# Optimization experiments

Hardware: AMD Instinct MI355X
Metric: run time of the kernel (lower is better)

## Reference

```python
import jax, jax.numpy as jnp
import numpy as np

B, N, M, D, F, L = 128, 512, 512, 256, 512, 5
EPS = 1e-5  # torch InstanceNorm1d default eps


def setup_inputs() -> dict:
    key = jax.random.key(0)
    ks = jax.random.split(key, 12)
    s_d = 1.0 / np.sqrt(D)
    s_f = 1.0 / np.sqrt(F)
    return {
        "row_emb": jax.random.normal(ks[0], (B, N, D), jnp.float32),
        "col_emb": jax.random.normal(ks[1], (B, M, D), jnp.float32),
        "cost_mat": jax.random.uniform(ks[2], (B, N, M), jnp.float32),
        "log_scale": jnp.float32(np.log2(N)),
        "Wq": jax.random.normal(ks[3], (L, 2, D, D), jnp.float32) * s_d,
        "Wk": jax.random.normal(ks[4], (L, 2, D, D), jnp.float32) * s_d,
        "Wv": jax.random.normal(ks[5], (L, 2, D, D), jnp.float32) * s_d,
        "g1": jnp.ones((L, 2, D), jnp.float32),
        "be1": jnp.zeros((L, 2, D), jnp.float32),
        "W1": jax.random.normal(ks[6], (L, 2, D, F), jnp.float32) * s_d,
        "b1": jnp.zeros((L, 2, F), jnp.float32),
        "W2": jax.random.normal(ks[7], (L, 2, F, D), jnp.float32) * s_f,
        "b2": jnp.zeros((L, 2, D), jnp.float32),
        "g2": jnp.ones((L, 2, D), jnp.float32),
        "be2": jnp.zeros((L, 2, D), jnp.float32),
        "alpha": jnp.ones((L, 2), jnp.float32),
    }


def _instance_norm(x, g, b):
    # x: (B, seq, D); normalize over seq per (batch, channel), affine over D
    mu = x.mean(axis=1, keepdims=True)
    var = jnp.mean(jnp.square(x - mu), axis=1, keepdims=True)
    return (x - mu) * jax.lax.rsqrt(var + EPS) * g + b


def _aft(q, k, v, adaptation_bias):
    # Attention-free mixing: exp(bias) shared across numerator/denominator GEMMs
    E = jnp.exp(adaptation_bias)          # (B, n, m)
    ek = jnp.exp(k)                       # (B, m, D)
    num = jnp.einsum('bnm,bmd->bnd', E, ek * v)
    den = jnp.einsum('bnm,bmd->bnd', E, ek)
    weighted = jnp.nan_to_num(num / den)  # matches torch nan/inf safety net
    return jax.nn.sigmoid(q) * weighted


def _enc_block(xr, xc, cm, Wq, Wk, Wv, g1, be1, W1, b1, W2, b2, g2, be2, alpha):
    q = xr @ Wq
    k = xc @ Wk
    v = xc @ Wv
    out_aft = _aft(q, k, v, alpha * cm)
    h1 = _instance_norm(xr + out_aft, g1, be1)
    ff = jax.nn.relu(h1 @ W1 + b1) @ W2 + b2
    return _instance_norm(h1 + ff, g2, be2)


def reference(row_emb, col_emb, cost_mat, log_scale, Wq, Wk, Wv,
              g1, be1, W1, b1, W2, b2, g2, be2, alpha):
    cm = (-log_scale) * cost_mat          # (B, N, M)
    cmT = jnp.swapaxes(cm, 1, 2)          # (B, M, N)
    for l in range(L):
        new_row = _enc_block(row_emb, col_emb, cm,
                             Wq[l, 0], Wk[l, 0], Wv[l, 0], g1[l, 0], be1[l, 0],
                             W1[l, 0], b1[l, 0], W2[l, 0], b2[l, 0],
                             g2[l, 0], be2[l, 0], alpha[l, 0])
        new_col = _enc_block(col_emb, row_emb, cmT,
                             Wq[l, 1], Wk[l, 1], Wv[l, 1], g1[l, 1], be1[l, 1],
                             W1[l, 1], b1[l, 1], W2[l, 1], b2[l, 1],
                             g2[l, 1], be2[l, 1], alpha[l, 1])
        row_emb, col_emb = new_row, new_col
    return (row_emb, col_emb)
```

## Files before the change

### kernel.cpp

```cpp
#include <hip/hip_runtime.h>

typedef unsigned short u16;
typedef __attribute__((ext_vector_type(8))) short short8;
typedef __attribute__((ext_vector_type(4))) float f32x4;

#define DEVFUN __device__ __forceinline__

namespace {

constexpr int kB = 128;
constexpr int kN = 512;
constexpr int kD = 256;
constexpr int kF = 512;
constexpr int kL = 5;
constexpr float kEPS = 1e-5f;
constexpr long BND = (long)kB * kN * kD;

DEVFUN float bf2f(u16 u) {
  unsigned v = ((unsigned)u) << 16;
  float f;
  __builtin_memcpy(&f, &v, 4);
  return f;
}
DEVFUN u16 f2bf(float f) {
  unsigned x;
  __builtin_memcpy(&x, &f, 4);
  x = (x + 0x7FFFu + ((x >> 16) & 1u)) >> 16;
  return (u16)x;
}
DEVFUN u16 f2h(float f) {
  _Float16 h = (_Float16)f;
  u16 u;
  __builtin_memcpy(&u, &h, 2);
  return u;
}
DEVFUN float h2f(u16 u) {
  _Float16 h;
  __builtin_memcpy(&h, &u, 2);
  return (float)h;
}
DEVFUN float fsig(float x) { return 1.f / (1.f + __expf(-x)); }

union Pk8 { u16 p[8]; uint4 v; };
union Pk4 { u16 p[4]; uint2 v; };

DEVFUN void gload16(const u16* g, u16* l) {
  __builtin_amdgcn_global_load_lds(
      (const __attribute__((address_space(1))) void*)g,
      (__attribute__((address_space(3))) void*)l, 16, 0, 0);
}

DEVFUN void waitv8() { asm volatile("s_waitcnt vmcnt(8)" ::: "memory"); }
DEVFUN void waitv0() { asm volatile("s_waitcnt vmcnt(0)" ::: "memory"); }

template <int MODE>
__global__ __launch_bounds__(256) void tcvt(const float* __restrict__ src,
                                            u16* __restrict__ dst, int R,
                                            int C, const float* __restrict__ al,
                                            int pi, const float* __restrict__ ls) {
  __shared__ u16 T[64 * 64];
  const int t = threadIdx.x;
  const long z = blockIdx.z;
  const int cBase = blockIdx.x * 64, rBase = blockIdx.y * 64;
  float s = 0.f;
  if constexpr (MODE == 1) s = -al[pi] * ls[0];
#pragma unroll
  for (int i = 0; i < 4; ++i) {
    int u = i * 256 + t;
    int n = u >> 4, m4 = u & 15;
    float4 v = *(const float4*)(src + (z * R + rBase + n) * C + cBase + m4 * 4);
    Pk4 pk;
    if constexpr (MODE == 1) {
      pk.p[0] = f2bf(__expf(s * v.x)); pk.p[1] = f2bf(__expf(s * v.y));
      pk.p[2] = f2bf(__expf(s * v.z)); pk.p[3] = f2bf(__expf(s * v.w));
    } else if constexpr (MODE == 2) {
      pk.p[0] = f2h(v.x); pk.p[1] = f2h(v.y);
      pk.p[2] = f2h(v.z); pk.p[3] = f2h(v.w);
    } else {
      pk.p[0] = f2bf(v.x); pk.p[1] = f2bf(v.y);
      pk.p[2] = f2bf(v.z); pk.p[3] = f2bf(v.w);
    }
    int ch = (m4 >> 1) ^ ((n >> 3) & 7), hf = m4 & 1;
    *(uint2*)&T[n * 64 + ch * 8 + hf * 4] = pk.v;
  }
  __syncthreads();
#pragma unroll
  for (int j = 0; j < 2; ++j) {
    int u = j * 256 + t;
    int om = u >> 3, nc = u & 7;
    Pk8 pk;
#pragma unroll
    for (int i = 0; i < 8; ++i) {
      int n = nc * 8 + i;
      int ch = (om >> 3) ^ ((n >> 3) & 7);
      pk.p[i] = T[n * 64 + ch * 8 + (om & 7)];
    }
    *(uint4*)(dst + (z * C + cBase + om) * R + rBase + nc * 8) = pk.v;
  }
}

__global__ __launch_bounds__(256) void eexp(const float* __restrict__ src,
                                            u16* __restrict__ dst, long n8,
                                            const float* __restrict__ al,
                                            int pi, const float* __restrict__ ls) {
  const float s = -al[pi] * ls[0];
  for (long i = blockIdx.x * 256 + threadIdx.x; i < n8;
       i += (long)gridDim.x * 256) {
    const float* p = src + i * 8;
    float4 v0 = *(const float4*)p, v1 = *(const float4*)(p + 4);
    Pk8 pk;
    pk.p[0] = f2bf(__expf(s * v0.x)); pk.p[1] = f2bf(__expf(s * v0.y));
    pk.p[2] = f2bf(__expf(s * v0.z)); pk.p[3] = f2bf(__expf(s * v0.w));
    pk.p[4] = f2bf(__expf(s * v1.x)); pk.p[5] = f2bf(__expf(s * v1.y));
    pk.p[6] = f2bf(__expf(s * v1.z)); pk.p[7] = f2bf(__expf(s * v1.w));
    *(uint4*)(dst + i * 8) = pk.v;
  }
}

__global__ __launch_bounds__(256) void eexpH(const u16* __restrict__ src,
                                             u16* __restrict__ dst, long n8,
                                             const float* __restrict__ al,
                                             int pi, const float* __restrict__ ls) {
  const float s = -al[pi] * ls[0];
  for (long i = blockIdx.x * 256 + threadIdx.x; i < n8;
       i += (long)gridDim.x * 256) {
    Pk8 h;
    h.v = *(const uint4*)(src + i * 8);
    Pk8 pk;
#pragma unroll
    for (int q = 0; q < 8; ++q) pk.p[q] = f2bf(__expf(s * h2f(h.p[q])));
    *(uint4*)(dst + i * 8) = pk.v;
  }
}

template <int MODE>
__global__ __launch_bounds__(256) void cvtb(const float* __restrict__ src,
                                            u16* __restrict__ dst, long n8) {
  for (long i = blockIdx.x * 256 + threadIdx.x; i < n8;
       i += (long)gridDim.x * 256) {
    const float* p = src + i * 8;
    float4 v0 = *(const float4*)p, v1 = *(const float4*)(p + 4);
    Pk8 pk;
    if constexpr (MODE == 2) {
      pk.p[0] = f2h(v0.x); pk.p[1] = f2h(v0.y);
      pk.p[2] = f2h(v0.z); pk.p[3] = f2h(v0.w);
      pk.p[4] = f2h(v1.x); pk.p[5] = f2h(v1.y);
      pk.p[6] = f2h(v1.z); pk.p[7] = f2h(v1.w);
    } else {
      pk.p[0] = f2bf(v0.x); pk.p[1] = f2bf(v0.y);
      pk.p[2] = f2bf(v0.z); pk.p[3] = f2bf(v0.w);
      pk.p[4] = f2bf(v1.x); pk.p[5] = f2bf(v1.y);
      pk.p[6] = f2bf(v1.z); pk.p[7] = f2bf(v1.w);
    }
    *(uint4*)(dst + i * 8) = pk.v;
  }
}

DEVFUN void mfma_step(const u16* As, const u16* Bs, int wr, int wc, int lr,
                      int lhi, f32x4 acc[4][4]) {
#pragma unroll
  for (int ks = 0; ks < 2; ++ks) {
    short8 af[4], bfr[4];
#pragma unroll
    for (int m = 0; m < 4; ++m) {
      int r = wr + m * 16 + lr;
      af[m] = *(const short8*)&As[r * 64 + (((ks << 2) + lhi) ^ (r & 7)) * 8];
    }
#pragma unroll
    for (int n = 0; n < 4; ++n) {
      int r = wc + n * 16 + lr;
      bfr[n] = *(const short8*)&Bs[r * 64 + (((ks << 2) + lhi) ^ (r & 7)) * 8];
    }
#pragma unroll
    for (int m = 0; m < 4; ++m)
#pragma unroll
      for (int n = 0; n < 4; ++n)
        acc[m][n] = __builtin_amdgcn_mfma_f32_16x16x32_bf16(af[m], bfr[n],
                                                            acc[m][n], 0, 0, 0);
  }
}

enum Epi { EP_SIG = 0, EP_RELUB, EP_BIASRES };

template <int EPI, int KK>
__global__ __launch_bounds__(256) void gemm_mf(
    const u16* __restrict__ Asrc, const u16* __restrict__ WT, int gx,
    void* __restrict__ outp, const void* __restrict__ aux,
    const u16* __restrict__ aux2b, float* __restrict__ statsF) {
  __shared__ u16 SM[4 * 8192];
  const int t = threadIdx.x;
  const int lane = t & 63, wid = t >> 6;
  const int lr = lane & 15, lhi = lane >> 4;
  const int wr = (wid >> 1) * 64, wc = (wid & 1) * 64;
  const int cpx = gridDim.x >> 3;
  const int rb = (blockIdx.x & 7) * cpx + (blockIdx.x >> 3);
  const int bx = rb % gx;
  const long rowBase = (long)(rb / gx) * 128;
  const int colBase = bx * 128;
  const int r0 = wid * 32;
  const int rl = lane >> 3, sl = lane & 7;

  f32x4 acc[4][4];
#pragma unroll
  for (int m = 0; m < 4; ++m)
#pragma unroll
    for (int n = 0; n < 4; ++n) acc[m][n] = {0.f, 0.f, 0.f, 0.f};

  auto stage = [&](int tt, int pb) {
    const int kt = tt << 6;
    u16* As = SM + pb * 16384;
    u16* Bs = SM + pb * 16384 + 8192;
#pragma unroll
    for (int j = 0; j < 4; ++j) {
      int r = r0 + j * 8 + rl;
      int gch = sl ^ (r & 7);
      gload16(Asrc + (rowBase + r) * KK + kt + gch * 8, &As[(r0 + j * 8) * 64]);
      gload16(WT + (long)(colBase + r) * KK + kt + gch * 8,
              &Bs[(r0 + j * 8) * 64]);
    }
  };

  constexpr int NT = KK >> 6;
  stage(0, 0);
  stage(1, 1);
  waitv8();
  __builtin_amdgcn_s_barrier();
#pragma unroll
  for (int tt = 0; tt < NT - 1; ++tt) {
    mfma_step(SM + (tt & 1) * 16384, SM + (tt & 1) * 16384 + 8192, wr, wc, lr,
              lhi, acc);
    __builtin_amdgcn_s_barrier();
    if (tt + 2 < NT) {
      stage(tt + 2, tt & 1);
      waitv8();
    } else {
      waitv0();
    }
    __builtin_amdgcn_s_barrier();
  }
  mfma_step(SM + ((NT - 1) & 1) * 16384, SM + ((NT - 1) & 1) * 16384 + 8192,
            wr, wc, lr, lhi, acc);

  float psum[4] = {0.f, 0.f, 0.f, 0.f}, psq[4] = {0.f, 0.f, 0.f, 0.f};
#pragma unroll
  for (int m = 0; m < 4; ++m) {
#pragma unroll
    for (int n = 0; n < 4; ++n) {
#pragma unroll
      for (int rr = 0; rr < 4; ++rr) {
        float v = acc[m][n][rr];
        long grow = rowBase + wr + m * 16 + lhi * 4 + rr;
        int gcol = colBase + wc + n * 16 + lr;
        if constexpr (EPI == EP_SIG) {
          ((u16*)outp)[grow * 256 + gcol] = f2bf(fsig(v));
        } else if constexpr (EPI == EP_RELUB) {
          float bb = ((const float*)aux)[gcol];
          ((u16*)outp)[grow * 512 + gcol] = f2bf(fmaxf(v + bb, 0.f));
        } else {
          float bb = ((const float*)aux)[gcol];
          float y = v + bb + bf2f(aux2b[grow * 256 + gcol]);
          ((u16*)outp)[grow * 256 + gcol] = f2bf(y);
          psum[n] += y;
          psq[n] += y * y;
        }
      }
    }
  }

  if constexpr (EPI == EP_BIASRES) {
    __syncthreads();
    float* stS = (float*)SM;
    float* stQ = stS + 8 * 128;
    const int ctr = (wid >> 1) * 4 + lhi;
#pragma unroll
    for (int n = 0; n < 4; ++n) {
      stS[ctr * 128 + wc + n * 16 + lr] = psum[n];
      stQ[ctr * 128 + wc + n * 16 + lr] = psq[n];
    }
    __syncthreads();
    if (t < 128) {
      float s = 0.f, q = 0.f;
#pragma unroll
      for (int i = 0; i < 8; ++i) {
        s += stS[i * 128 + t];
        q += stQ[i * 128 + t];
      }
      const long b = rowBase >> 9;
      const int rblk = (int)((rowBase >> 7) & 3);
      const long o = ((b * 4 + rblk) * 256 + colBase + t) * 2;
      statsF[o] = s;
      statsF[o + 1] = q;
    }
  }
}

union KvSm {
  struct { u16 A[128 * 64]; u16 Bk[128 * 64]; u16 Bv[128 * 64]; } s;
  u16 T[128 * 128];
};

__global__ __launch_bounds__(256) void kv_mf(const u16* __restrict__ Asrc,
                                             const u16* __restrict__ WkT,
                                             const u16* __restrict__ WvT,
                                             u16* __restrict__ Cb) {
  __shared__ KvSm sm;
  const int t = threadIdx.x;
  const int lane = t & 63, wid = t >> 6;
  const int lr = lane & 15, lhi = lane >> 4;
  const int wr = (wid >> 1) * 64, wc = (wid & 1) * 64;
  const int cpx = gridDim.x >> 3;
  const int rb = (blockIdx.x & 7) * cpx + (blockIdx.x >> 3);
  const long rowBase = (long)(rb >> 1) * 128;
  const int colBase = (rb & 1) * 128;
  const long b = rowBase >> 9;
  const int mInB = (int)(rowBase & 511);
  const int r0 = wid * 32;
  const int rl = lane >> 3, sl = lane & 7;

  f32x4 ka[4][4], va[4][4];
#pragma unroll
  for (int m = 0; m < 4; ++m)
#pragma unroll
    for (int n = 0; n < 4; ++n) {
      ka[m][n] = {0.f, 0.f, 0.f, 0.f};
      va[m][n] = {0.f, 0.f, 0.f, 0.f};
    }

  for (int kt = 0; kt < 256; kt += 64) {
#pragma unroll
    for (int j = 0; j < 4; ++j) {
      int r = r0 + j * 8 + rl;
      int gch = sl ^ (r & 7);
      gload16(Asrc + (rowBase + r) * 256 + kt + gch * 8,
              &sm.s.A[(r0 + j * 8) * 64]);
      gload16(WkT + (long)(colBase + r) * 256 + kt + gch * 8,
              &sm.s.Bk[(r0 + j * 8) * 64]);
      gload16(WvT + (long)(colBase + r) * 256 + kt + gch * 8,
              &sm.s.Bv[(r0 + j * 8) * 64]);
    }
    __syncthreads();
    mfma_step(sm.s.A, sm.s.Bk, wr, wc, lr, lhi, ka);
    mfma_step(sm.s.A, sm.s.Bv, wr, wc, lr, lhi, va);
    __syncthreads();
  }

#pragma unroll
  for (int pass = 0; pass < 2; ++pass) {
#pragma unroll
    for (int m = 0; m < 4; ++m) {
#pragma unroll
      for (int n = 0; n < 4; ++n) {
        int m0 = wr + m * 16 + lhi * 4;
        int d = wc + n * 16 + lr;
        Pk4 pk;
#pragma unroll
        for (int rr = 0; rr < 4; ++rr) {
          float ek = __expf(ka[m][n][rr]);
          pk.p[rr] = f2bf(pass ? ek * va[m][n][rr] : ek);
        }
        int slot = (m0 >> 3) ^ (d & 7);
        *(uint2*)&sm.T[d * 128 + slot * 8 + (m0 & 7)] = pk.v;
      }
    }
    __syncthreads();
    const long rbase = b * 512 + (pass ? 0 : 256) + colBase;
#pragma unroll
    for (int j = 0; j < 8; ++j) {
      int idx = j * 256 + t;
      int d = idx >> 4, c = idx & 15;
      uint4 v = *(const uint4*)&sm.T[d * 128 + ((c ^ (d & 7)) * 8)];
      *(uint4*)(Cb + (rbase + d) * 512 + mInB + c * 8) = v;
    }
    __syncthreads();
  }
}

union SmU {
  struct { u16 A[128 * 64]; u16 B[128 * 64]; } s;
  struct { float den[128 * 68]; float st[2][8][64]; } d;
};

__global__ __launch_bounds__(256) void aft_mf(
    const u16* __restrict__ Ebuf, const u16* __restrict__ CbufT,
    const u16* __restrict__ qb, const u16* __restrict__ xrB,
    u16* __restrict__ dst, float* __restrict__ statsF) {
  __shared__ SmU sm;
  const int t = threadIdx.x;
  const int lane = t & 63, wid = t >> 6;
  const int lr = lane & 15, lhi = lane >> 4;
  const int wr = (wid >> 1) * 64, wc = (wid & 1) * 64;
  const int rb = (blockIdx.x & 7) * 256 + (blockIdx.x >> 3);
  const long b = rb >> 4;
  const int nBase = ((rb >> 2) & 3) * 128;
  const int dBase = (rb & 3) * 64;
  const int r0 = wid * 32;
  const int rl = lane >> 3, sl = lane & 7;

  f32x4 acc[4][4];
#pragma unroll
  for (int m = 0; m < 4; ++m)
#pragma unroll
    for (int n = 0; n < 4; ++n) acc[m][n] = {0.f, 0.f, 0.f, 0.f};

  for (int kt = 0; kt < 512; kt += 64) {
#pragma unroll
    for (int j = 0; j < 4; ++j) {
      int r = r0 + j * 8 + rl;
      int gch = sl ^ (r & 7);
      gload16(Ebuf + (b * 512 + nBase + r) * 512 + kt + gch * 8,
              &sm.s.A[(r0 + j * 8) * 64]);
      int gslot = (r < 64) ? (dBase + r) : (256 + dBase + (r - 64));
      gload16(CbufT + (b * 512 + gslot) * 512 + kt + gch * 8,
              &sm.s.B[(r0 + j * 8) * 64]);
    }
    __syncthreads();
    mfma_step(sm.s.A, sm.s.B, wr, wc, lr, lhi, acc);
    __syncthreads();
  }

  if (wc == 64) {
#pragma unroll
    for (int m = 0; m < 4; ++m)
#pragma unroll
      for (int n = 0; n < 4; ++n)
#pragma unroll
        for (int rr = 0; rr < 4; ++rr) {
          int nl = wr + m * 16 + lhi * 4 + rr;
          int dl = n * 16 + lr;
          sm.d.den[nl * 68 + dl] = acc[m][n][rr];
        }
  }
  __syncthreads();
  float psum[4] = {0.f, 0.f, 0.f, 0.f}, psq[4] = {0.f, 0.f, 0.f, 0.f};
  if (wc == 0) {
#pragma unroll
    for (int m = 0; m < 4; ++m)
#pragma unroll
      for (int n = 0; n < 4; ++n)
#pragma unroll
        for (int rr = 0; rr < 4; ++rr) {
          int nl = wr + m * 16 + lhi * 4 + rr;
          int dl = n * 16 + lr;
          float dv = sm.d.den[nl * 68 + dl];
          float w = acc[m][n][rr] / dv;
          if (!(w == w)) w = 0.f;
          else if (w > 3.402823466e38f) w = 3.402823466e38f;
          else if (w < -3.402823466e38f) w = -3.402823466e38f;
          long grow = b * 512 + nBase + nl;
          int gcol = dBase + dl;
          float sq = bf2f(qb[grow * 256 + gcol]);
          float y = bf2f(xrB[grow * 256 + gcol]) + sq * w;
          dst[grow * 256 + gcol] = f2bf(y);
          psum[n] += y;
          psq[n] += y * y;
        }
  }
  __syncthreads();
  if (wc == 0) {
    const int ctr = (wid >> 1) * 4 + lhi;
#pragma unroll
    for (int n = 0; n < 4; ++n) {
      sm.d.st[0][ctr][n * 16 + lr] = psum[n];
      sm.d.st[1][ctr][n * 16 + lr] = psq[n];
    }
  }
  __syncthreads();
  if (t < 64) {
    float s = 0.f, q = 0.f;
#pragma unroll
    for (int i = 0; i < 8; ++i) {
      s += sm.d.st[0][i][t];
      q += sm.d.st[1][i][t];
    }
    const long o = ((b * 4 + (nBase >> 7)) * 256 + dBase + t) * 2;
    statsF[o] = s;
    statsF[o + 1] = q;
  }
}

template <bool LASTF32>
__global__ __launch_bounds__(256) void inormS(const u16* __restrict__ Xin,
                                              const float* __restrict__ stats,
                                              const float* __restrict__ g,
                                              const float* __restrict__ be,
                                              u16* __restrict__ Xb,
                                              float* __restrict__ Xf) {
  const int b = blockIdx.x;
  const int ch0 = blockIdx.y * 64;
  const int nlo = blockIdx.z * 256;
  const int t = threadIdx.x;
  const int lc = t & 63;
  const int ch = ch0 + lc;
  const int nr = t >> 6;
  const long base = (long)b * kN * kD + ch;

  __shared__ float s1[4][64], s2[4][64];
  __shared__ float mu[64], rs[64], gg[64], bb[64];
  {
    const long o = (((long)b * 4 + nr) * 256 + ch) * 2;
    s1[nr][lc] = stats[o];
    s2[nr][lc] = stats[o + 1];
  }
  __syncthreads();
  if (t < 64) {
    float ssum = s1[0][t] + s1[1][t] + s1[2][t] + s1[3][t];
    float ssq = s2[0][t] + s2[1][t] + s2[2][t] + s2[3][t];
    float m = ssum * (1.f / kN);
    float v = ssq * (1.f / kN) - m * m;
    mu[t] = m;
    rs[t] = rsqrtf(v + kEPS);
    gg[t] = g[ch0 + t];
    bb[t] = be[ch0 + t];
  }
  __syncthreads();
  const float m = mu[lc], rr = rs[lc], G = gg[lc], Bt = bb[lc];
  for (int n = nlo + nr; n < nlo + 256; n += 4) {
    long idx = base + (long)n * kD;
    float y = (bf2f(Xin[idx]) - m) * rr * G + Bt;
    Xb[idx] = f2bf(y);
    if constexpr (LASTF32) Xf[idx] = y;
  }
}

}

extern "C" void kernel_launch(void* const* d_in, const int* in_sizes, int n_in,
                              void* d_out, int out_size, void* d_ws,
                              size_t ws_size, hipStream_t stream) {
  (void)in_sizes; (void)n_in; (void)out_size;

  const float* in_row = (const float*)d_in[0];
  const float* in_col = (const float*)d_in[1];
  const float* cost = (const float*)d_in[2];
  const float* lsc = (const float*)d_in[3];
  const float* Wq = (const float*)d_in[4];
  const float* Wk = (const float*)d_in[5];
  const float* Wv = (const float*)d_in[6];
  const float* g1 = (const float*)d_in[7];
  const float* be1 = (const float*)d_in[8];
  const float* W1 = (const float*)d_in[9];
  const float* b1 = (const float*)d_in[10];
  const float* W2 = (const float*)d_in[11];
  const float* b2 = (const float*)d_in[12];
  const float* g2 = (const float*)d_in[13];
  const float* be2 = (const float*)d_in[14];
  const float* alpha = (const float*)d_in[15];

  float* outRow = (float*)d_out;
  float* outCol = outRow + BND;

  u16* qb = (u16*)d_ws;
  u16* h1b = qb;
  u16* CbufT = qb + BND;
  u16* ffmid = CbufT;
  u16* Ebuf = CbufT + 2 * BND;
  u16* bSt = Ebuf + 2 * BND;
  u16* h0b = bSt + 4 * BND;
  u16* h2b = h0b;
  u16* WqT = h0b + BND;
  u16* WkT = WqT + 10L * 256 * 256;
  u16* WvT = WkT + 10L * 256 * 256;
  u16* W1T = WvT + 10L * 256 * 256;
  u16* W2T = W1T + 10L * 512 * 256;
  float* statsF = (float*)(W2T + 10L * 256 * 512);
  u16* costTH = (u16*)(statsF + 128L * 4 * 256 * 2);
  u16* costH = costTH + 2 * BND;
  const long needElems = (long)(costH - (u16*)d_ws) + 2 * BND;
  const bool haveCH = (long)ws_size >= needElems * 2;

  const dim3 blk(256);
  tcvt<0><<<dim3(4, 4, 10), blk, 0, stream>>>(Wq, WqT, 256, 256, nullptr, 0, nullptr);
  tcvt<0><<<dim3(4, 4, 10), blk, 0, stream>>>(Wk, WkT, 256, 256, nullptr, 0, nullptr);
  tcvt<0><<<dim3(4, 4, 10), blk, 0, stream>>>(Wv, WvT, 256, 256, nullptr, 0, nullptr);
  tcvt<0><<<dim3(8, 4, 10), blk, 0, stream>>>(W1, W1T, 256, 512, nullptr, 0, nullptr);
  tcvt<0><<<dim3(4, 8, 10), blk, 0, stream>>>(W2, W2T, 512, 256, nullptr, 0, nullptr);
  cvtb<0><<<1024, blk, 0, stream>>>(in_row, bSt + 0 * BND, BND / 8);
  cvtb<0><<<1024, blk, 0, stream>>>(in_col, bSt + 1 * BND, BND / 8);
  if (haveCH) {
    tcvt<2><<<dim3(8, 8, 128), blk, 0, stream>>>(cost, costTH, 512, 512,
                                                 nullptr, 0, nullptr);
    cvtb<2><<<2048, blk, 0, stream>>>(cost, costH, 2 * BND / 8);
  }

  for (int l = 0; l < kL; ++l) {
    const int inPar = l & 1, outPar = 1 - inPar;
    const u16* bR = bSt + (inPar * 2 + 0) * BND;
    const u16* bC = bSt + (inPar * 2 + 1) * BND;

    for (int side = 0; side < 2; ++side) {
      const u16* xrB = side ? bC : bR;
      const u16* xcB = side ? bR : bC;
      u16* outB = bSt + (outPar * 2 + side) * BND;
      float* outF = side ? outCol : outRow;
      const int pi = l * 2 + side;

      if (side == 0) {
        if (haveCH)
          eexpH<<<4096, blk, 0, stream>>>(costH, Ebuf, 2 * BND / 8, alpha, pi,
                                          lsc);
        else
          eexp<<<4096, blk, 0, stream>>>(cost, Ebuf, 2 * BND / 8, alpha, pi,
                                         lsc);
      } else if (haveCH) {
        eexpH<<<4096, blk, 0, stream>>>(costTH, Ebuf, 2 * BND / 8, alpha, pi,
                                        lsc);
      } else {
        tcvt<1><<<dim3(8, 8, 128), blk, 0, stream>>>(cost, Ebuf, 512, 512,
                                                     alpha, pi, lsc);
      }

      gemm_mf<EP_SIG, 256><<<1024, blk, 0, stream>>>(
          xrB, WqT + (long)pi * 256 * 256, 2, qb, nullptr, nullptr, nullptr);
      kv_mf<<<1024, blk, 0, stream>>>(xcB, WkT + (long)pi * 256 * 256,
                                      WvT + (long)pi * 256 * 256, CbufT);
      aft_mf<<<2048, blk, 0, stream>>>(Ebuf, CbufT, qb, xrB, h0b, statsF);
      inormS<false><<<dim3(128, 4, 2), blk, 0, stream>>>(
          h0b, statsF, g1 + pi * 256, be1 + pi * 256, h1b, nullptr);
      gemm_mf<EP_RELUB, 256><<<2048, blk, 0, stream>>>(
          h1b, W1T + (long)pi * 512 * 256, 4, ffmid, b1 + pi * 512, nullptr,
          nullptr);
      gemm_mf<EP_BIASRES, 512><<<1024, blk, 0, stream>>>(
          ffmid, W2T + (long)pi * 256 * 512, 2, h2b, b2 + pi * 256, h1b,
          statsF);
      if (l == kL - 1)
        inormS<true><<<dim3(128, 4, 2), blk, 0, stream>>>(
            h2b, statsF, g2 + pi * 256, be2 + pi * 256, outB, outF);
      else
        inormS<false><<<dim3(128, 4, 2), blk, 0, stream>>>(
            h2b, statsF, g2 + pi * 256, be2 + pi * 256, outB, nullptr);
    }
  }
}
```

Baseline: 3.220 ms.

## Batch row and column encoder sides into single dual-problem kernel launches

Each kernel (exp of cost, Q GEMM, KV GEMM, AFT, instance norms, FFN GEMMs) now takes two sets of pointers and splits its grid so one launch processes both the row and column sides of a layer. Separate workspace buffers are allocated for the second side when the workspace is large enough. This halves the number of launches and doubles grid size, reducing tail effects and launch gaps. The cost is higher workspace use and some extra selection logic per block.

```diff
diff --git a/kernel.cpp b/kernel.cpp
--- a/kernel.cpp
+++ b/kernel.cpp
@@ -124,6 +124,31 @@
   const float s = -al[pi] * ls[0];
   for (long i = blockIdx.x * 256 + threadIdx.x; i < n8;
        i += (long)gridDim.x * 256) {
+    Pk8 h;
+    h.v = *(const uint4*)(src + i * 8);
+    Pk8 pk;
+#pragma unroll
+    for (int q = 0; q < 8; ++q) pk.p[q] = f2bf(__expf(s * h2f(h.p[q])));
+    *(uint4*)(dst + i * 8) = pk.v;
+  }
+}
+
+__global__ __launch_bounds__(256) void eexp2H(const u16* __restrict__ src0,
+                                              u16* __restrict__ dst0,
+                                              const u16* __restrict__ src1,
+                                              u16* __restrict__ dst1,
+                                              const float* __restrict__ al,
+                                              int pi0, int pi1,
+                                              const float* __restrict__ ls) {
+  const int half = gridDim.x >> 1;
+  const bool sd1 = (int)blockIdx.x >= half;
+  const int sbid = sd1 ? blockIdx.x - half : blockIdx.x;
+  const u16* src = sd1 ? src1 : src0;
+  u16* dst = sd1 ? dst1 : dst0;
+  const float s = -al[sd1 ? pi1 : pi0] * ls[0];
+  const long n8 = 2 * BND / 8;
+  const long stride = (long)half * 256;
+  for (long i = (long)sbid * 256 + threadIdx.x; i < n8; i += stride) {
     Pk8 h;
     h.v = *(const uint4*)(src + i * 8);
     Pk8 pk;
@@ -184,16 +209,27 @@
 
 template <int EPI, int KK>
 __global__ __launch_bounds__(256) void gemm_mf(
-    const u16* __restrict__ Asrc, const u16* __restrict__ WT, int gx,
-    void* __restrict__ outp, const void* __restrict__ aux,
-    const u16* __restrict__ aux2b, float* __restrict__ statsF) {
+    const u16* __restrict__ A0, const u16* __restrict__ WT0, void* out0,
+    const void* aux0, const u16* __restrict__ res0, float* st0,
+    const u16* __restrict__ A1, const u16* __restrict__ WT1, void* out1,
+    const void* aux1, const u16* __restrict__ res1, float* st1, int gx,
+    int half) {
   __shared__ u16 SM[4 * 8192];
+  const bool sd1 = (int)blockIdx.x >= half;
+  const int sbid = sd1 ? blockIdx.x - half : blockIdx.x;
+  const u16* Asrc = sd1 ? A1 : A0;
+  const u16* WT = sd1 ? WT1 : WT0;
+  void* outp = sd1 ? out1 : out0;
+  const void* aux = sd1 ? aux1 : aux0;
+  const u16* aux2b = sd1 ? res1 : res0;
+  float* statsF = sd1 ? st1 : st0;
+
   const int t = threadIdx.x;
   const int lane = t & 63, wid = t >> 6;
   const int lr = lane & 15, lhi = lane >> 4;
   const int wr = (wid >> 1) * 64, wc = (wid & 1) * 64;
-  const int cpx = gridDim.x >> 3;
-  const int rb = (blockIdx.x & 7) * cpx + (blockIdx.x >> 3);
+  const int cpx = half >> 3;
+  const int rb = (sbid & 7) * cpx + (sbid >> 3);
   const int bx = rb % gx;
   const long rowBase = (long)(rb / gx) * 128;
   const int colBase = bx * 128;
@@ -299,17 +335,25 @@
   u16 T[128 * 128];
 };
 
-__global__ __launch_bounds__(256) void kv_mf(const u16* __restrict__ Asrc,
-                                             const u16* __restrict__ WkT,
-                                             const u16* __restrict__ WvT,
-                                             u16* __restrict__ Cb) {
+__global__ __launch_bounds__(256) void kv_mf(
+    const u16* __restrict__ A0, const u16* __restrict__ Wk0,
+    const u16* __restrict__ Wv0, u16* __restrict__ Cb0,
+    const u16* __restrict__ A1, const u16* __restrict__ Wk1,
+    const u16* __restrict__ Wv1, u16* __restrict__ Cb1, int half) {
   __shared__ KvSm sm;
+  const bool sd1 = (int)blockIdx.x >= half;
+  const int sbid = sd1 ? blockIdx.x - half : blockIdx.x;
+  const u16* Asrc = sd1 ? A1 : A0;
+  const u16* WkT = sd1 ? Wk1 : Wk0;
+  const u16* WvT = sd1 ? Wv1 : Wv0;
+  u16* Cb = sd1 ? Cb1 : Cb0;
+
   const int t = threadIdx.x;
   const int lane = t & 63, wid = t >> 6;
   const int lr = lane & 15, lhi = lane >> 4;
   const int wr = (wid >> 1) * 64, wc = (wid & 1) * 64;
-  const int cpx = gridDim.x >> 3;
-  const int rb = (blockIdx.x & 7) * cpx + (blockIdx.x >> 3);
+  const int cpx = half >> 3;
+  const int rb = (sbid & 7) * cpx + (sbid >> 3);
   const long rowBase = (long)(rb >> 1) * 128;
   const int colBase = (rb & 1) * 128;
   const long b = rowBase >> 9;
@@ -381,15 +425,27 @@
 };
 
 __global__ __launch_bounds__(256) void aft_mf(
-    const u16* __restrict__ Ebuf, const u16* __restrict__ CbufT,
-    const u16* __restrict__ qb, const u16* __restrict__ xrB,
-    u16* __restrict__ dst, float* __restrict__ statsF) {
+    const u16* __restrict__ E0, const u16* __restrict__ C0,
+    const u16* __restrict__ q0, const u16* __restrict__ x0,
+    u16* __restrict__ d0, float* s0, const u16* __restrict__ E1,
+    const u16* __restrict__ C1, const u16* __restrict__ q1,
+    const u16* __restrict__ x1, u16* __restrict__ d1, float* s1, int half) {
   __shared__ SmU sm;
+  const bool sd1 = (int)blockIdx.x >= half;
+  const int sbid = sd1 ? blockIdx.x - half : blockIdx.x;
+  const u16* Ebuf = sd1 ? E1 : E0;
+  const u16* CbufT = sd1 ? C1 : C0;
+  const u16* qb = sd1 ? q1 : q0;
+  const u16* xrB = sd1 ? x1 : x0;
+  u16* dst = sd1 ? d1 : d0;
+  float* statsF = sd1 ? s1 : s0;
+
   const int t = threadIdx.x;
   const int lane = t & 63, wid = t >> 6;
   const int lr = lane & 15, lhi = lane >> 4;
   const int wr = (wid >> 1) * 64, wc = (wid & 1) * 64;
-  const int rb = (blockIdx.x & 7) * 256 + (blockIdx.x >> 3);
+  const int cpx = half >> 3;
+  const int rb = (sbid & 7) * cpx + (sbid >> 3);
   const long b = rb >> 4;
   const int nBase = ((rb >> 2) & 3) * 128;
   const int dBase = (rb & 3) * 64;
@@ -479,15 +535,25 @@
 }
 
 template <bool LASTF32>
-__global__ __launch_bounds__(256) void inormS(const u16* __restrict__ Xin,
-                                              const float* __restrict__ stats,
-                                              const float* __restrict__ g,
-                                              const float* __restrict__ be,
-                                              u16* __restrict__ Xb,
-                                              float* __restrict__ Xf) {
+__global__ __launch_bounds__(256) void inormS(
+    const u16* __restrict__ X0, const float* __restrict__ st0,
+    const float* __restrict__ g0, const float* __restrict__ be0,
+    u16* __restrict__ Xb0, float* __restrict__ Xf0,
+    const u16* __restrict__ X1, const float* __restrict__ st1,
+    const float* __restrict__ g1_, const float* __restrict__ be1_,
+    u16* __restrict__ Xb1, float* __restrict__ Xf1, int zHalf) {
+  const bool sd1 = (int)blockIdx.z >= zHalf;
+  const int zz = sd1 ? blockIdx.z - zHalf : blockIdx.z;
+  const u16* Xin = sd1 ? X1 : X0;
+  const float* stats = sd1 ? st1 : st0;
+  const float* g = sd1 ? g1_ : g0;
+  const float* be = sd1 ? be1_ : be0;
+  u16* Xb = sd1 ? Xb1 : Xb0;
+  float* Xf = sd1 ? Xf1 : Xf0;
+
   const int b = blockIdx.x;
   const int ch0 = blockIdx.y * 64;
-  const int nlo = blockIdx.z * 256;
+  const int nlo = zz * 256;
   const int t = threadIdx.x;
   const int lc = t & 63;
   const int ch = ch0 + lc;
@@ -550,23 +616,27 @@
   float* outCol = outRow + BND;
 
   u16* qb = (u16*)d_ws;
-  u16* h1b = qb;
   u16* CbufT = qb + BND;
-  u16* ffmid = CbufT;
   u16* Ebuf = CbufT + 2 * BND;
   u16* bSt = Ebuf + 2 * BND;
   u16* h0b = bSt + 4 * BND;
-  u16* h2b = h0b;
   u16* WqT = h0b + BND;
   u16* WkT = WqT + 10L * 256 * 256;
   u16* WvT = WkT + 10L * 256 * 256;
   u16* W1T = WvT + 10L * 256 * 256;
   u16* W2T = W1T + 10L * 512 * 256;
   float* statsF = (float*)(W2T + 10L * 256 * 512);
-  u16* costTH = (u16*)(statsF + 128L * 4 * 256 * 2);
+  float* statsF1 = statsF + 128L * 4 * 256 * 2;
+  u16* costTH = (u16*)(statsF1 + 128L * 4 * 256 * 2);
   u16* costH = costTH + 2 * BND;
-  const long needElems = (long)(costH - (u16*)d_ws) + 2 * BND;
-  const bool haveCH = (long)ws_size >= needElems * 2;
+  u16* qb1 = costH + 2 * BND;
+  u16* CbufT1 = qb1 + BND;
+  u16* Ebuf1 = CbufT1 + 2 * BND;
+  u16* h0b1 = Ebuf1 + 2 * BND;
+  const long needCH = (long)(costH + 2 * BND - (u16*)d_ws);
+  const long needDual = (long)(h0b1 + BND - (u16*)d_ws);
+  const bool haveCH = (long)ws_size >= needCH * 2;
+  const bool haveDual = (long)ws_size >= needDual * 2;
 
   const dim3 blk(256);
   tcvt<0><<<dim3(4, 4, 10), blk, 0, stream>>>(Wq, WqT, 256, 256, nullptr, 0, nullptr);
@@ -586,11 +656,50 @@
     const int inPar = l & 1, outPar = 1 - inPar;
     const u16* bR = bSt + (inPar * 2 + 0) * BND;
     const u16* bC = bSt + (inPar * 2 + 1) * BND;
+    u16* outB0 = bSt + (outPar * 2 + 0) * BND;
+    u16* outB1 = bSt + (outPar * 2 + 1) * BND;
+    const int pi0 = l * 2, pi1 = l * 2 + 1;
+
+    if (haveDual) {
+      eexp2H<<<8192, blk, 0, stream>>>(costH, Ebuf, costTH, Ebuf1, alpha, pi0,
+                                       pi1, lsc);
+      gemm_mf<EP_SIG, 256><<<2048, blk, 0, stream>>>(
+          bR, WqT + (long)pi0 * 65536, qb, nullptr, nullptr, nullptr, bC,
+          WqT + (long)pi1 * 65536, qb1, nullptr, nullptr, nullptr, 2, 1024);
+      kv_mf<<<2048, blk, 0, stream>>>(bC, WkT + (long)pi0 * 65536,
+                                      WvT + (long)pi0 * 65536, CbufT, bR,
+                                      WkT + (long)pi1 * 65536,
+                                      WvT + (long)pi1 * 65536, CbufT1, 1024);
+      aft_mf<<<4096, blk, 0, stream>>>(Ebuf, CbufT, qb, bR, h0b, statsF,
+                                       Ebuf1, CbufT1, qb1, bC, h0b1, statsF1,
+                                       2048);
+      inormS<false><<<dim3(128, 4, 4), blk, 0, stream>>>(
+          h0b, statsF, g1 + pi0 * 256, be1 + pi0 * 256, qb, nullptr, h0b1,
+          statsF1, g1 + pi1 * 256, be1 + pi1 * 256, qb1, nullptr, 2);
+      gemm_mf<EP_RELUB, 256><<<4096, blk, 0, stream>>>(
+          qb, W1T + (long)pi0 * 131072, CbufT, b1 + pi0 * 512, nullptr,
+          nullptr, qb1, W1T + (long)pi1 * 131072, CbufT1, b1 + pi1 * 512,
+          nullptr, nullptr, 4, 2048);
+      gemm_mf<EP_BIASRES, 512><<<2048, blk, 0, stream>>>(
+          CbufT, W2T + (long)pi0 * 131072, h0b, b2 + pi0 * 256, qb, statsF,
+          CbufT1, W2T + (long)pi1 * 131072, h0b1, b2 + pi1 * 256, qb1,
+          statsF1, 2, 1024);
+      if (l == kL - 1)
+        inormS<true><<<dim3(128, 4, 4), blk, 0, stream>>>(
+            h0b, statsF, g2 + pi0 * 256, be2 + pi0 * 256, outB0, outRow, h0b1,
+            statsF1, g2 + pi1 * 256, be2 + pi1 * 256, outB1, outCol, 2);
+      else
+        inormS<false><<<dim3(128, 4, 4), blk, 0, stream>>>(
+            h0b, statsF, g2 + pi0 * 256, be2 + pi0 * 256, outB0, nullptr,
+            h0b1, statsF1, g2 + pi1 * 256, be2 + pi1 * 256, outB1, nullptr,
+            2);
+      continue;
+    }
 
     for (int side = 0; side < 2; ++side) {
       const u16* xrB = side ? bC : bR;
       const u16* xcB = side ? bR : bC;
-      u16* outB = bSt + (outPar * 2 + side) * BND;
+      u16* outB = side ? outB1 : outB0;
       float* outF = side ? outCol : outRow;
       const int pi = l * 2 + side;
 
@@ -610,24 +719,33 @@
       }
 
       gemm_mf<EP_SIG, 256><<<1024, blk, 0, stream>>>(
-          xrB, WqT + (long)pi * 256 * 256, 2, qb, nullptr, nullptr, nullptr);
-      kv_mf<<<1024, blk, 0, stream>>>(xcB, WkT + (long)pi * 256 * 256,
-                                      WvT + (long)pi * 256 * 256, CbufT);
-      aft_mf<<<2048, blk, 0, stream>>>(Ebuf, CbufT, qb, xrB, h0b, statsF);
+          xrB, WqT + (long)pi * 65536, qb, nullptr, nullptr, nullptr, xrB,
+          WqT + (long)pi * 65536, qb, nullptr, nullptr, nullptr, 2, 1024);
+      kv_mf<<<1024, blk, 0, stream>>>(
+          xcB, WkT + (long)pi * 65536, WvT + (long)pi * 65536, CbufT, xcB,
+          WkT + (long)pi * 65536, WvT + (long)pi * 65536, CbufT, 1024);
+      aft_mf<<<2048, blk, 0, stream>>>(Ebuf, CbufT, qb, xrB, h0b, statsF,
+                                       Ebuf, CbufT, qb, xrB, h0b, statsF,
+                                       2048);
       inormS<false><<<dim3(128, 4, 2), blk, 0, stream>>>(
-          h0b, statsF, g1 + pi * 256, be1 + pi * 256, h1b, nullptr);
+          h0b, statsF, g1 + pi * 256, be1 + pi * 256, qb, nullptr, h0b,
+          statsF, g1 + pi * 256, be1 + pi * 256, qb, nullptr, 2);
       gemm_mf<EP_RELUB, 256><<<2048, blk, 0, stream>>>(
-          h1b, W1T + (long)pi * 512 * 256, 4, ffmid, b1 + pi * 512, nullptr,
-          nullptr);
+          qb, W1T + (long)pi * 131072, CbufT, b1 + pi * 512, nullptr, nullptr,
+          qb, W1T + (long)pi * 131072, CbufT, b1 + pi * 512, nullptr, nullptr,
+          4, 2048);
       gemm_mf<EP_BIASRES, 512><<<1024, blk, 0, stream>>>(
-          ffmid, W2T + (long)pi * 256 * 512, 2, h2b, b2 + pi * 256, h1b,
-          statsF);
+          CbufT, W2T + (long)pi * 131072, h0b, b2 + pi * 256, qb, statsF,
+          CbufT, W2T + (long)pi * 131072, h0b, b2 + pi * 256, qb, statsF, 2,
+          1024);
       if (l == kL - 1)
         inormS<true><<<dim3(128, 4, 2), blk, 0, stream>>>(
-            h2b, statsF, g2 + pi * 256, be2 + pi * 256, outB, outF);
+            h0b, statsF, g2 + pi * 256, be2 + pi * 256, outB, outF, h0b,
+            statsF, g2 + pi * 256, be2 + pi * 256, outB, outF, 2);
       else
         inormS<false><<<dim3(128, 4, 2), blk, 0, stream>>>(
-            h2b, statsF, g2 + pi * 256, be2 + pi * 256, outB, nullptr);
-    }
-  }
-}
+            h0b, statsF, g2 + pi * 256, be2 + pi * 256, outB, nullptr, h0b,
+            statsF, g2 + pi * 256, be2 + pi * 256, outB, nullptr, 2);
+    }
+  }
+}
```

Measured after the change: 3.362 ms. 1.04x slower.

## Widen AFT tile to 128 d-columns with 512-thread blocks to reuse E tile

Applied to the files above, without the earlier changes.

The AFT kernel now covers 128 output channels per block (numerator and denominator, 256 B-rows) with 8 waves, halving the grid. Each E tile loaded from global memory is reused across twice as many channels, which cuts the dominant E-matrix traffic in half. The epilogue is split into two phases to fit the denominator staging into the smaller shared buffer. The cost is more shared memory and registers per block, extra barriers, and fewer blocks for scheduling.

```diff
diff --git a/kernel.cpp b/kernel.cpp
--- a/kernel.cpp
+++ b/kernel.cpp
@@ -375,25 +375,21 @@
   }
 }
 
-union SmU {
-  struct { u16 A[128 * 64]; u16 B[128 * 64]; } s;
-  struct { float den[128 * 68]; float st[2][8][64]; } d;
-};
-
-__global__ __launch_bounds__(256) void aft_mf(
+__global__ __launch_bounds__(512) void aft_mf(
     const u16* __restrict__ Ebuf, const u16* __restrict__ CbufT,
     const u16* __restrict__ qb, const u16* __restrict__ xrB,
     u16* __restrict__ dst, float* __restrict__ statsF) {
-  __shared__ SmU sm;
+  __shared__ u16 SM[24576];
+  u16* const As = SM;
+  u16* const Bs = SM + 8192;
   const int t = threadIdx.x;
   const int lane = t & 63, wid = t >> 6;
   const int lr = lane & 15, lhi = lane >> 4;
-  const int wr = (wid >> 1) * 64, wc = (wid & 1) * 64;
-  const int rb = (blockIdx.x & 7) * 256 + (blockIdx.x >> 3);
-  const long b = rb >> 4;
-  const int nBase = ((rb >> 2) & 3) * 128;
-  const int dBase = (rb & 3) * 64;
-  const int r0 = wid * 32;
+  const int wn = wid >> 2, wq = wid & 3;
+  const int rb = (blockIdx.x & 7) * 128 + (blockIdx.x >> 3);
+  const long b = rb >> 3;
+  const int nBase = ((rb >> 1) & 3) * 128;
+  const int dBase = (rb & 1) * 128;
   const int rl = lane >> 3, sl = lane & 7;
 
   f32x4 acc[4][4];
@@ -404,73 +400,87 @@
 
   for (int kt = 0; kt < 512; kt += 64) {
 #pragma unroll
-    for (int j = 0; j < 4; ++j) {
-      int r = r0 + j * 8 + rl;
-      int gch = sl ^ (r & 7);
-      gload16(Ebuf + (b * 512 + nBase + r) * 512 + kt + gch * 8,
-              &sm.s.A[(r0 + j * 8) * 64]);
-      int gslot = (r < 64) ? (dBase + r) : (256 + dBase + (r - 64));
-      gload16(CbufT + (b * 512 + gslot) * 512 + kt + gch * 8,
-              &sm.s.B[(r0 + j * 8) * 64]);
-    }
-    __syncthreads();
-    mfma_step(sm.s.A, sm.s.B, wr, wc, lr, lhi, acc);
-    __syncthreads();
-  }
-
-  if (wc == 64) {
-#pragma unroll
-    for (int m = 0; m < 4; ++m)
-#pragma unroll
-      for (int n = 0; n < 4; ++n)
-#pragma unroll
-        for (int rr = 0; rr < 4; ++rr) {
-          int nl = wr + m * 16 + lhi * 4 + rr;
-          int dl = n * 16 + lr;
-          sm.d.den[nl * 68 + dl] = acc[m][n][rr];
-        }
+    for (int j = 0; j < 6; ++j) {
+      int c = wid * 6 + j;
+      if (c < 16) {
+        int r = c * 8 + rl;
+        int gch = sl ^ (r & 7);
+        gload16(Ebuf + (b * 512 + nBase + r) * 512 + kt + gch * 8,
+                &As[c * 512]);
+      } else {
+        int rbl = (c - 16) * 8 + rl;
+        int gch = sl ^ (rbl & 7);
+        int gslot = (rbl < 128) ? (dBase + rbl) : (256 + dBase + (rbl - 128));
+        gload16(CbufT + (b * 512 + gslot) * 512 + kt + gch * 8,
+                &Bs[(c - 16) * 512]);
+      }
+    }
+    __syncthreads();
+    mfma_step(As, Bs, wn * 64, wq * 64, lr, lhi, acc);
+    __syncthreads();
+  }
+
+  const bool isNum = (wq < 2);
+  float* const den = (float*)SM;
+  float psum[4] = {0.f, 0.f, 0.f, 0.f}, psq[4] = {0.f, 0.f, 0.f, 0.f};
+#pragma unroll
+  for (int ph = 0; ph < 2; ++ph) {
+    __syncthreads();
+    if (wn == ph && !isNum) {
+#pragma unroll
+      for (int m = 0; m < 4; ++m)
+#pragma unroll
+        for (int n = 0; n < 4; ++n)
+#pragma unroll
+          for (int rr = 0; rr < 4; ++rr) {
+            int rowl = m * 16 + lhi * 4 + rr;
+            int dl = (wq - 2) * 64 + n * 16 + lr;
+            den[rowl * 132 + dl] = acc[m][n][rr];
+          }
+    }
+    __syncthreads();
+    if (wn == ph && isNum) {
+#pragma unroll
+      for (int m = 0; m < 4; ++m)
+#pragma unroll
+        for (int n = 0; n < 4; ++n)
+#pragma unroll
+          for (int rr = 0; rr < 4; ++rr) {
+            int rowl = m * 16 + lhi * 4 + rr;
+            int dl = wq * 64 + n * 16 + lr;
+            float dv = den[rowl * 132 + dl];
+            float w = acc[m][n][rr] / dv;
+            if (!(w == w)) w = 0.f;
+            else if (w > 3.402823466e38f) w = 3.402823466e38f;
+            else if (w < -3.402823466e38f) w = -3.402823466e38f;
+            long grow = b * 512 + nBase + wn * 64 + rowl;
+            int gcol = dBase + dl;
+            float sq = bf2f(qb[grow * 256 + gcol]);
+            float y = bf2f(xrB[grow * 256 + gcol]) + sq * w;
+            dst[grow * 256 + gcol] = f2bf(y);
+            psum[n] += y;
+            psq[n] += y * y;
+          }
+    }
   }
   __syncthreads();
-  float psum[4] = {0.f, 0.f, 0.f, 0.f}, psq[4] = {0.f, 0.f, 0.f, 0.f};
-  if (wc == 0) {
-#pragma unroll
-    for (int m = 0; m < 4; ++m)
-#pragma unroll
-      for (int n = 0; n < 4; ++n)
-#pragma unroll
-        for (int rr = 0; rr < 4; ++rr) {
-          int nl = wr + m * 16 + lhi * 4 + rr;
-          int dl = n * 16 + lr;
-          float dv = sm.d.den[nl * 68 + dl];
-          float w = acc[m][n][rr] / dv;
-          if (!(w == w)) w = 0.f;
-          else if (w > 3.402823466e38f) w = 3.402823466e38f;
-          else if (w < -3.402823466e38f) w = -3.402823466e38f;
-          long grow = b * 512 + nBase + nl;
-          int gcol = dBase + dl;
-          float sq = bf2f(qb[grow * 256 + gcol]);
-          float y = bf2f(xrB[grow * 256 + gcol]) + sq * w;
-          dst[grow * 256 + gcol] = f2bf(y);
-          psum[n] += y;
-          psq[n] += y * y;
-        }
+  float* const stS = (float*)SM;
+  float* const stQ = stS + 8 * 128;
+  if (isNum) {
+    const int ctr = wn * 4 + lhi;
+#pragma unroll
+    for (int n = 0; n < 4; ++n) {
+      stS[ctr * 128 + wq * 64 + n * 16 + lr] = psum[n];
+      stQ[ctr * 128 + wq * 64 + n * 16 + lr] = psq[n];
+    }
   }
   __syncthreads();
-  if (wc == 0) {
-    const int ctr = (wid >> 1) * 4 + lhi;
-#pragma unroll
-    for (int n = 0; n < 4; ++n) {
-      sm.d.st[0][ctr][n * 16 + lr] = psum[n];
-      sm.d.st[1][ctr][n * 16 + lr] = psq[n];
-    }
-  }
-  __syncthreads();
-  if (t < 64) {
+  if (t < 128) {
     float s = 0.f, q = 0.f;
 #pragma unroll
     for (int i = 0; i < 8; ++i) {
-      s += sm.d.st[0][i][t];
-      q += sm.d.st[1][i][t];
+      s += stS[i * 128 + t];
+      q += stQ[i * 128 + t];
     }
     const long o = ((b * 4 + (nBase >> 7)) * 256 + dBase + t) * 2;
     statsF[o] = s;
@@ -568,7 +578,7 @@
   const long needElems = (long)(costH - (u16*)d_ws) + 2 * BND;
   const bool haveCH = (long)ws_size >= needElems * 2;
 
-  const dim3 blk(256);
+  const dim3 blk(256), blk5(512);
   tcvt<0><<<dim3(4, 4, 10), blk, 0, stream>>>(Wq, WqT, 256, 256, nullptr, 0, nullptr);
   tcvt<0><<<dim3(4, 4, 10), blk, 0, stream>>>(Wk, WkT, 256, 256, nullptr, 0, nullptr);
   tcvt<0><<<dim3(4, 4, 10), blk, 0, stream>>>(Wv, WvT, 256, 256, nullptr, 0, nullptr);
@@ -613,7 +623,7 @@
           xrB, WqT + (long)pi * 256 * 256, 2, qb, nullptr, nullptr, nullptr);
       kv_mf<<<1024, blk, 0, stream>>>(xcB, WkT + (long)pi * 256 * 256,
                                       WvT + (long)pi * 256 * 256, CbufT);
-      aft_mf<<<2048, blk, 0, stream>>>(Ebuf, CbufT, qb, xrB, h0b, statsF);
+      aft_mf<<<1024, blk5, 0, stream>>>(Ebuf, CbufT, qb, xrB, h0b, statsF);
       inormS<false><<<dim3(128, 4, 2), blk, 0, stream>>>(
           h0b, statsF, g1 + pi * 256, be1 + pi * 256, h1b, nullptr);
       gemm_mf<EP_RELUB, 256><<<2048, blk, 0, stream>>>(
```

Result: slower. 3.657 ms (+13.6%).
